# Performance work log

Measured on AMD Instinct MI355X. Metric: run time of the kernel, lower is better.

The kernel has to match this reference:

```python
import jax, jax.numpy as jnp
import numpy as np

N, A, MO, LX, H, S, P, B, BL = 64, 128, 126, 96, 1024, 32, 2, 16, 32
T = (B - 2) * BL
L = B * BL        # 512
IN = MO + A + LX + S      # 382: cat([mo, aud, lxm, style])
GIN = IN + H              # 1406: GRU input = cat([in_embed, mo, aud, lxm, style])

def gelu(x):
    return jax.nn.gelu(x, approximate=False)  # torch F.gelu default (erf)

def gru_cell(x, h, wih, whh, bih, bhh):
    # torch nn.GRU cell math
    gi = x @ wih + bih  # [N,3H]
    gh = h @ whh + bhh  # [N,3H]
    ir, iz, inn = jnp.split(gi, 3, axis=-1)
    hr, hz, hn = jnp.split(gh, 3, axis=-1)
    r = jax.nn.sigmoid(ir + hr)
    z = jax.nn.sigmoid(iz + hz)
    n = jnp.tanh(inn + r * hn)
    return (1.0 - z) * n + z * h

def layernorm(x, g, b, eps=1e-5):
    m = x.mean(-1, keepdims=True)
    v = x.var(-1, keepdims=True)
    return (x - m) * jax.lax.rsqrt(v + eps) * g + b

def setup_inputs():
    key = jax.random.key(0)
    k = jax.random.split(key, 20)
    f = jnp.float32
    def rn(i, shape, s=0.05):
        return jax.random.normal(k[i], shape, dtype=f) * s
    return dict(
        aud_embed=jax.random.normal(k[0], (N, A, T), f),
        mo=jax.random.normal(k[1], (N, MO, L), f),
        lxm=jax.random.normal(k[2], (N, LX, B), f),
        vid_indices=jax.random.randint(k[3], (N, B), 0, 5),
        eps=jax.random.normal(k[4], (T, N, S), f),
        csi_w0=rn(5, (MO + LX, H)), csi_b0=jnp.zeros((H,), f),
        csi_w1=rn(6, (H, H)), csi_b1=jnp.zeros((H,), f),
        csi_w2=rn(7, (H, H * P)), csi_b2=jnp.zeros((H * P,), f),
        spk_emb=rn(8, (5, S), 0.001),
        mu_w=rn(9, (S, S)), mu_b=jnp.zeros((S,), f),
        lv_w=rn(10, (S, S)), lv_b=jnp.zeros((S,), f),
        emb_in_w=rn(11, (IN, H)), emb_in_b=jnp.zeros((H,), f),
        wih0=rn(12, (GIN, 3 * H)), whh0=rn(13, (H, 3 * H)),
        bih0=jnp.zeros((3 * H,), f), bhh0=jnp.zeros((3 * H,), f),
        wih1=rn(14, (H, 3 * H)), whh1=rn(15, (H, 3 * H)),
        bih1=jnp.zeros((3 * H,), f), bhh1=jnp.zeros((3 * H,), f),
        ln_g=jnp.ones((H,), f), ln_b=jnp.zeros((H,), f),
        pred_w=rn(16, (H, MO), 0.02), pred_b=jnp.zeros((MO,), f),
    )

def reference(aud_embed, mo, lxm, vid_indices, eps,
              csi_w0, csi_b0, csi_w1, csi_b1, csi_w2, csi_b2,
              spk_emb, mu_w, mu_b, lv_w, lv_b,
              emb_in_w, emb_in_b,
              wih0, whh0, bih0, bhh0, wih1, whh1, bih1, bhh1,
              ln_g, ln_b, pred_w, pred_b):
    # CellStateInitializer(mo[:,:,BL-1], lxm[:,:,0]) -> [P, N, H]
    x = gelu(jnp.concatenate([mo[:, :, BL - 1], lxm[:, :, 0]], axis=-1) @ csi_w0 + csi_b0)
    x = gelu(x @ csi_w1 + csi_b1)
    x = (x @ csi_w2 + csi_b2).reshape(N, P, H)
    cell = jnp.transpose(x, (1, 0, 2))  # [P,N,H]

    blk = jnp.repeat(jnp.arange(B - 2), BL)            # [T] block index per frame
    aud_seq = jnp.transpose(aud_embed, (2, 0, 1))      # [T,N,A]
    lxm_seq = jnp.transpose(lxm, (2, 0, 1))[blk + 1]   # [T,N,LX]
    vid_seq = vid_indices.T[blk + 1]                   # [T,N]
    zc = spk_emb[vid_seq]                              # [T,N,S]
    z_mu = zc @ mu_w + mu_b                            # [T,N,S]
    z_lv = zc @ lv_w + lv_b                            # [T,N,S]
    style = z_mu + eps * jnp.exp(0.5 * z_lv)           # reparameterize, fresh eps each frame

    def step(carry, xs):
        pre_mo, h0, h1 = carry
        aud_t, lxm_t, st_t = xs
        xcat = jnp.concatenate([pre_mo, aud_t, lxm_t, st_t], axis=-1)  # [N,IN]
        ine = gelu(xcat @ emb_in_w + emb_in_b)                          # [N,H]
        gx = jnp.concatenate([ine, xcat], axis=-1)                      # [N,GIN]
        h0n = gru_cell(gx, h0, wih0, whh0, bih0, bhh0)
        h1n = gru_cell(h0n, h1, wih1, whh1, bih1, bhh1)
        out = layernorm(h1n, ln_g, ln_b)
        pred = out @ pred_w + pred_b                                    # [N,MO]
        return (pred, h0n, h1n), pred

    init = (mo[:, :, BL - 1], cell[0], cell[1])
    _, preds = jax.lax.scan(step, init, (aud_seq, lxm_seq, style))
    mo_hat = jnp.transpose(preds, (1, 2, 0))   # [N,MO,T]
    z_mu_hat = jnp.transpose(z_mu, (1, 2, 0))  # [N,S,T]
    z_lv_hat = jnp.transpose(z_lv, (1, 2, 0))  # [N,S,T]
    return mo_hat, z_mu_hat, z_lv_hat
```

## Files before the change

### kernel.cpp

```cpp
#include <hip/hip_runtime.h>
#include <cmath>

typedef _Float16 f16;
typedef _Float16 f16x8 __attribute__((ext_vector_type(8)));
typedef float f32x4 __attribute__((ext_vector_type(4)));
typedef unsigned long long u64;

#define MFMA_F16(a,b,c) __builtin_amdgcn_mfma_f32_16x16x32_f16((a),(b),(c),0,0,0)
#define AGENT __HIP_MEMORY_SCOPE_AGENT

#define TSTEPS 448
#define OFF_MU 3612672
#define OFF_LV 4530176
#define LDS_BYTES 156160

#define S1 0
#define S2 1
#define S3 2
#define S3B 3
#define S4 4
#define S4G 5

struct Ptrs {
  const float *aud, *mo, *lxm, *eps;
  const int *vid;
  const float *csi_w0, *csi_b0, *csi_w1, *csi_b1, *csi_w2, *csi_b2;
  const float *spk, *mu_w, *mu_b, *lv_w, *lv_b;
  const float *embW, *embB;
  const float *wih0, *whh0, *bih0, *bhh0;
  const float *wih1, *whh1, *bih1, *bhh1;
  const float *ln_g, *ln_b, *predW, *predB;
  float *out;
  unsigned *bar;
  float *part, *mu5, *lv5, *h0F, *h1F, *gsbs;
  f16 *h0B, *h1B, *ineB, *xcat;
  float *ghP0, *ghP1, *x0, *x1, *predsT;
  f16 *whh0P, *whh1P, *wih0aP, *wih0bP, *wih1P, *embWP, *predWP;
};

__device__ __forceinline__ float geluf(float x) {
  return 0.5f * x * (1.0f + erff(x * 0.7071067811865475f));
}
__device__ __forceinline__ float sigmf(float x) {
  return __builtin_amdgcn_rcpf(1.0f + __expf(-x));
}
__device__ __forceinline__ float tanhf_fast(float x) {
  float xc = fmaxf(x, -44.f);
  float e = __expf(-2.f * xc);
  return (1.f - e) * __builtin_amdgcn_rcpf(1.f + e);
}

__device__ __forceinline__ u64 ldc8(const void* p) {
  return __hip_atomic_load((const u64*)p, __ATOMIC_RELAXED, AGENT);
}
__device__ __forceinline__ void stc8(void* p, u64 v) {
  __hip_atomic_store((u64*)p, v, __ATOMIC_RELAXED, AGENT);
}
__device__ __forceinline__ void stcf(float* p, float v) {
  __hip_atomic_store(p, v, __ATOMIC_RELAXED, AGENT);
}
__device__ __forceinline__ f16x8 toH(u64 a, u64 b) {
  union { u64 u[2]; f16x8 h; } r; r.u[0] = a; r.u[1] = b; return r.h;
}
__device__ __forceinline__ f32x4 toF(u64 a, u64 b) {
  union { u64 u[2]; f32x4 f; } r; r.u[0] = a; r.u[1] = b; return r.f;
}
__device__ __forceinline__ u64 packF2(float a, float b) {
  union { float f[2]; u64 u; } r; r.f[0] = a; r.f[1] = b; return r.u;
}
__device__ __forceinline__ void st_pair(f16* base, float v, int lm, bool pred) {
  float vn = __shfl_xor(v, 1);
  if (!(lm & 1) && pred) {
    union { f16 h[2]; unsigned u; } pk;
    pk.h[0] = (f16)v; pk.h[1] = (f16)vn;
    __hip_atomic_store((unsigned*)base, pk.u, __ATOMIC_RELAXED, AGENT);
  }
}


__global__ void k_init(Ptrs p) {
  int gid = blockIdx.x * 256 + threadIdx.x;
  if (gid < 16384) p.bar[gid] = 0u;
}

__global__ void k_pack(const float* __restrict__ src, f16* __restrict__ dst,
                       int K, int rowOff, int realN, int ldN,
                       const float* __restrict__ scale) {
  int ct = blockIdx.x, kt = blockIdx.y;
  int e = threadIdx.x * 2;
  int l = e >> 3, i = e & 7;
  int k = kt * 32 + (l >> 4) * 8 + i;
  int col = ct * 16 + (l & 15);
  f16 v0 = (f16)0.f, v1 = (f16)0.f;
  if (k < K && col < realN) {
    float s = scale ? scale[rowOff + k] : 1.f;
    v0 = (f16)(src[(size_t)(rowOff + k) * ldN + col] * s);
  }
  if (k + 1 < K && col < realN) {
    float s = scale ? scale[rowOff + k + 1] : 1.f;
    v1 = (f16)(src[(size_t)(rowOff + k + 1) * ldN + col] * s);
  }
  size_t o = ((size_t)ct * gridDim.y + kt) * 512 + e;
  dst[o] = v0; dst[o + 1] = v1;
}

__global__ void k_gsbs(Ptrs p) {
  int c = threadIdx.x;
  if (c < 126) {
    float gs = 0.f, bs = 0.f;
    for (int k = 0; k < 1024; k++) {
      float w = p.predW[(size_t)k * 126 + c];
      gs += p.ln_g[k] * w;
      bs += p.ln_b[k] * w;
    }
    p.gsbs[c] = gs; p.gsbs[128 + c] = bs;
  }
}

__global__ void k_csi1(Ptrs p) {
  int gid = blockIdx.x * 256 + threadIdx.x;
  int n = gid >> 10, c = gid & 1023;
  float acc = p.csi_b0[c];
  const float* w = p.csi_w0 + c;
  for (int k = 0; k < 126; k++) acc += p.mo[((size_t)(n * 126 + k)) * 512 + 31] * w[(size_t)k * 1024];
  for (int k = 0; k < 96; k++)  acc += p.lxm[(size_t)(n * 96 + k) * 16] * w[(size_t)(126 + k) * 1024];
  p.x0[gid] = geluf(acc);
}

__global__ void k_csi2(Ptrs p) {
  int gid = blockIdx.x * 256 + threadIdx.x;
  int n = gid >> 10, c = gid & 1023;
  float acc = p.csi_b1[c];
  const float* w = p.csi_w1 + c;
  const float* x = p.x0 + (size_t)n * 1024;
  for (int k = 0; k < 1024; k++) acc += x[k] * w[(size_t)k * 1024];
  p.x1[gid] = geluf(acc);
}

__global__ void k_csi3(Ptrs p) {
  int gid = blockIdx.x * 256 + threadIdx.x;
  int n = gid >> 11, c2 = gid & 2047;
  float acc = p.csi_b2[c2];
  const float* w = p.csi_w2 + c2;
  const float* x = p.x1 + (size_t)n * 1024;
  for (int k = 0; k < 1024; k++) acc += x[k] * w[(size_t)k * 2048];
  if (c2 < 1024) { p.h0F[n * 1024 + c2] = acc; p.h0B[n * 1024 + c2] = (f16)acc; }
  else           { p.h1F[n * 1024 + c2 - 1024] = acc; p.h1B[n * 1024 + c2 - 1024] = (f16)acc; }
}

__global__ void k_gh(Ptrs p) {
  int gid = blockIdx.x * 256 + threadIdx.x;
  int which = gid >= 196608;
  int g2 = which ? gid - 196608 : gid;
  int n = g2 / 3072, c = g2 % 3072;
  const float* h = which ? p.h1F : p.h0F;
  const float* W = which ? p.whh1 : p.whh0;
  const float* bb = which ? p.bhh1 : p.bhh0;
  float acc = bb[c];
  const float* hr = h + (size_t)n * 1024;
  for (int k = 0; k < 1024; k++) acc += hr[k] * W[(size_t)k * 3072 + c];
  int g = c >> 10, col = c & 1023;
  int ct = col >> 4, lm = col & 15, w = n >> 4, lq = (n >> 2) & 3, r = n & 3;
  float* dst = which ? p.ghP1 : p.ghP0;
  dst[((size_t)((ct * 16 + lm) * 16 + w * 4 + lq)) * 16 + g * 4 + r] = acc;
}

__global__ void k_style1(Ptrs p) {
  int tid = threadIdx.x;
  if (tid < 160) {
    int v = tid >> 5, s = tid & 31;
    float m = p.mu_b[s], lv = p.lv_b[s];
    for (int k = 0; k < 32; k++) {
      float z = p.spk[v * 32 + k];
      m += z * p.mu_w[k * 32 + s];
      lv += z * p.lv_w[k * 32 + s];
    }
    p.mu5[v * 32 + s] = m; p.lv5[v * 32 + s] = lv;
  }
}

__global__ void k_style2(Ptrs p) {
  int gid = blockIdx.x * 256 + threadIdx.x;
  int t = gid % 448;
  int rr = gid / 448;
  int s = rr & 31, n = rr >> 5;
  int v = p.vid[n * 16 + (t >> 5) + 1];
  float mu = p.mu5[v * 32 + s], lv = p.lv5[v * 32 + s];
  float e = p.eps[((size_t)t * 64 + n) * 32 + s];
  float st = mu + e * expf(0.5f * lv);
  p.out[OFF_MU + ((size_t)n * 32 + s) * 448 + t] = mu;
  p.out[OFF_LV + ((size_t)n * 32 + s) * 448 + t] = lv;
  p.xcat[((size_t)t * 64 + n) * 384 + 350 + s] = (f16)st;
}

__global__ void k_aud(Ptrs p) {
  __shared__ float tile[32][65];
  int bid = blockIdx.x;
  int n = bid / 28, rem = bid % 28;
  int a0 = (rem / 7) * 32, t0 = (rem % 7) * 64;
  int tid = threadIdx.x;
  for (int i = tid; i < 2048; i += 256) {
    int ai = i >> 6, tj = i & 63;
    tile[ai][tj] = p.aud[((size_t)n * 128 + a0 + ai) * 448 + t0 + tj];
  }
  __syncthreads();
  for (int i = tid; i < 2048; i += 256) {
    int tj = i >> 5, ai = i & 31;
    p.xcat[((size_t)(t0 + tj) * 64 + n) * 384 + 126 + a0 + ai] = (f16)tile[ai][tj];
  }
}

__global__ void k_lxm(Ptrs p) {
  int gid = blockIdx.x * 256 + threadIdx.x;
  int l_ = gid % 96;
  int r = gid / 96;
  int n = r & 63, t = r >> 6;
  int tb = (t >> 5) + 1;
  p.xcat[((size_t)t * 64 + n) * 384 + 254 + l_] = (f16)p.lxm[((size_t)n * 96 + l_) * 16 + tb];
}

__global__ void k_premo0(Ptrs p) {
  int gid = blockIdx.x * 256 + threadIdx.x;
  if (gid < 8064) {
    int n = gid / 126, m = gid % 126;
    p.xcat[(size_t)n * 384 + m] = (f16)p.mo[((size_t)n * 126 + m) * 512 + 31];
  }
}

__global__ void k_padz(Ptrs p) {
  int gid = blockIdx.x * 256 + threadIdx.x;
  int t = gid >> 7, rem = gid & 127;
  int n = rem >> 1, c = 382 + (rem & 1);
  p.xcat[((size_t)t * 64 + n) * 384 + c] = (f16)0.f;
}


__device__ __forceinline__ void sigc(unsigned* bar, int cls, int idx, unsigned val) {
  asm volatile("s_waitcnt vmcnt(0)" ::: "memory");
  __syncthreads();
  if (threadIdx.x == 0)
    __hip_atomic_store(&bar[(cls * 64 + idx) * 32], val, __ATOMIC_RELAXED, AGENT);
}
__device__ __forceinline__ void waitc(unsigned* bar, int cls, unsigned tgt, int nsig) {
  if (threadIdx.x < (unsigned)nsig) {
    const unsigned* f = &bar[(cls * 64 + threadIdx.x) * 32];
    while (__hip_atomic_load(f, __ATOMIC_RELAXED, AGENT) < tgt) {}
  }
  __syncthreads();
}

__device__ __forceinline__ void gemm3(const f16* aRow, const f16* L, int l,
                                      f32x4& A0, f32x4& A1, f32x4& A2) {
  const f16* w0 = L + l * 8;
  u64 ua[16], ub[16];
  #pragma unroll
  for (int j = 0; j < 8; j++) { ua[2*j] = ldc8(aRow + j * 32); ua[2*j+1] = ldc8(aRow + j * 32 + 4); }
  #pragma unroll
  for (int j = 0; j < 8; j++) { ub[2*j] = ldc8(aRow + 256 + j * 32); ub[2*j+1] = ldc8(aRow + 256 + j * 32 + 4); }
  #pragma unroll
  for (int j = 0; j < 8; j++) {
    f16x8 av = toH(ua[2*j], ua[2*j+1]);
    A0 = MFMA_F16(av, *(const f16x8*)(w0 + j * 512), A0);
    A1 = MFMA_F16(av, *(const f16x8*)(w0 + 16384 + j * 512), A1);
    A2 = MFMA_F16(av, *(const f16x8*)(w0 + 32768 + j * 512), A2);
  }
  #pragma unroll
  for (int j = 0; j < 8; j++) { ua[2*j] = ldc8(aRow + 512 + j * 32); ua[2*j+1] = ldc8(aRow + 512 + j * 32 + 4); }
  #pragma unroll
  for (int j = 0; j < 8; j++) {
    f16x8 av = toH(ub[2*j], ub[2*j+1]);
    int kt = 8 + j;
    A0 = MFMA_F16(av, *(const f16x8*)(w0 + kt * 512), A0);
    A1 = MFMA_F16(av, *(const f16x8*)(w0 + 16384 + kt * 512), A1);
    A2 = MFMA_F16(av, *(const f16x8*)(w0 + 32768 + kt * 512), A2);
  }
  #pragma unroll
  for (int j = 0; j < 8; j++) { ub[2*j] = ldc8(aRow + 768 + j * 32); ub[2*j+1] = ldc8(aRow + 768 + j * 32 + 4); }
  #pragma unroll
  for (int j = 0; j < 8; j++) {
    f16x8 av = toH(ua[2*j], ua[2*j+1]);
    int kt = 16 + j;
    A0 = MFMA_F16(av, *(const f16x8*)(w0 + kt * 512), A0);
    A1 = MFMA_F16(av, *(const f16x8*)(w0 + 16384 + kt * 512), A1);
    A2 = MFMA_F16(av, *(const f16x8*)(w0 + 32768 + kt * 512), A2);
  }
  #pragma unroll
  for (int j = 0; j < 8; j++) {
    f16x8 av = toH(ub[2*j], ub[2*j+1]);
    int kt = 24 + j;
    A0 = MFMA_F16(av, *(const f16x8*)(w0 + kt * 512), A0);
    A1 = MFMA_F16(av, *(const f16x8*)(w0 + 16384 + kt * 512), A1);
    A2 = MFMA_F16(av, *(const f16x8*)(w0 + 32768 + kt * 512), A2);
  }
}

__global__ __launch_bounds__(256, 1) void k_scan(Ptrs p) {
  extern __shared__ char smem[];
  f16* L = (f16*)smem;
  const int b = blockIdx.x, tid = threadIdx.x;
  const int w = tid >> 6, l = tid & 63;
  const int lm = l & 15, lq = l >> 4;

  {
    auto cp = [&](int dstF16, const f16* src, int nF16) {
      uint4* d = (uint4*)smem + (dstF16 >> 3);
      const uint4* s = (const uint4*)src;
      for (int i = tid; i < (nF16 >> 3); i += 256) d[i] = s[i];
    };
    if (b < 64) {
      cp(0,     p.wih0aP + (size_t)b * 16384, 16384);
      cp(16384, p.wih0aP + (size_t)(64 + b) * 16384, 16384);
      cp(32768, p.wih0aP + (size_t)(128 + b) * 16384, 16384);
      cp(49152, p.wih0bP + (size_t)b * 6144, 6144);
      cp(55296, p.wih0bP + (size_t)(64 + b) * 6144, 6144);
      cp(61440, p.wih0bP + (size_t)(128 + b) * 6144, 6144);
    } else if (b < 128) {
      int cb = b - 64;
      cp(0,     p.wih1P + (size_t)cb * 16384, 16384);
      cp(16384, p.wih1P + (size_t)(64 + cb) * 16384, 16384);
      cp(32768, p.wih1P + (size_t)(128 + cb) * 16384, 16384);
      cp(49152, p.embWP + (size_t)cb * 6144, 6144);
      if (cb < 8) cp(55296, p.predWP + (size_t)cb * 16384, 16384);
    } else if (b < 192) {
      int i = b - 128;
      cp(0,     p.whh0P + (size_t)i * 16384, 16384);
      cp(16384, p.whh0P + (size_t)(64 + i) * 16384, 16384);
      cp(32768, p.whh0P + (size_t)(128 + i) * 16384, 16384);
    } else {
      int i = b - 192;
      cp(0,     p.whh1P + (size_t)i * 16384, 16384);
      cp(16384, p.whh1P + (size_t)(64 + i) * 16384, 16384);
      cp(32768, p.whh1P + (size_t)(128 + i) * 16384, 16384);
    }
  }
  float b0r = 0.f, b1r = 0.f, b2r = 0.f, ebr = 0.f, pbr = 0.f;
  float GsR = 0.f, BsR = 0.f;
  float hs[4] = {0.f, 0.f, 0.f, 0.f};
  if (b < 64) {
    int col = b * 16 + lm;
    b0r = p.bih0[col]; b1r = p.bih0[1024 + col]; b2r = p.bih0[2048 + col];
    #pragma unroll
    for (int r = 0; r < 4; r++) hs[r] = p.h0F[(size_t)(w * 16 + lq * 4 + r) * 1024 + col];
  } else if (b < 128) {
    int col = (b - 64) * 16 + lm;
    b0r = p.bih1[col]; b1r = p.bih1[1024 + col]; b2r = p.bih1[2048 + col];
    ebr = p.embB[col];
    #pragma unroll
    for (int r = 0; r < 4; r++) hs[r] = p.h1F[(size_t)(w * 16 + lq * 4 + r) * 1024 + col];
    if (b < 72 && col < 126) {
      pbr = p.predB[col];
      GsR = p.gsbs[col];
      BsR = p.gsbs[128 + col];
    }
  } else if (b < 192) {
    int col = (b - 128) * 16 + lm;
    b0r = p.bhh0[col]; b1r = p.bhh0[1024 + col]; b2r = p.bhh0[2048 + col];
  } else {
    int col = (b - 192) * 16 + lm;
    b0r = p.bhh1[col]; b1r = p.bhh1[1024 + col]; b2r = p.bhh1[2048 + col];
  }
  __syncthreads();

  unsigned* bar = p.bar;

  for (unsigned t = 0; t < TSTEPS; t++) {
    const f16* xc = p.xcat + (size_t)t * 24576;

    if (b < 64) {
      f32x4 a0 = {0,0,0,0}, a1 = {0,0,0,0}, a2 = {0,0,0,0};
      const f16* aB = xc + (w * 16 + lm) * 384 + lq * 8;
      const f16* wl = L + 49152 + l * 8;
      #pragma unroll
      for (int kt = 4; kt < 12; kt++) {
        f16x8 av = *(const f16x8*)(aB + kt * 32);
        a0 = MFMA_F16(av, *(const f16x8*)(wl + kt * 512), a0);
        a1 = MFMA_F16(av, *(const f16x8*)(wl + 6144 + kt * 512), a1);
        a2 = MFMA_F16(av, *(const f16x8*)(wl + 12288 + kt * 512), a2);
      }
      if (t) waitc(bar, S4, t, 8);
      f32x4 gip0, gip1, gip2;
      {
        u64 up[8];
        #pragma unroll
        for (int kt = 0; kt < 4; kt++) { up[2*kt] = ldc8(aB + kt * 32); up[2*kt+1] = ldc8(aB + kt * 32 + 4); }
        #pragma unroll
        for (int kt = 0; kt < 4; kt++) {
          f16x8 av = toH(up[2*kt], up[2*kt+1]);
          a0 = MFMA_F16(av, *(const f16x8*)(wl + kt * 512), a0);
          a1 = MFMA_F16(av, *(const f16x8*)(wl + 6144 + kt * 512), a1);
          a2 = MFMA_F16(av, *(const f16x8*)(wl + 12288 + kt * 512), a2);
        }
        #pragma unroll
        for (int r = 0; r < 4; r++) {
          gip0[r] = a0[r] + b0r; gip1[r] = a1[r] + b1r; gip2[r] = a2[r] + b2r;
        }
      }
      waitc(bar, S3B, t, 64);
      const float* rec = p.ghP0 + ((size_t)((b * 16 + lm) * 16 + w * 4 + lq)) * 16;
      u64 r0 = ldc8(rec), r1 = ldc8(rec + 2), r2 = ldc8(rec + 4);
      u64 r3 = ldc8(rec + 6), r4 = ldc8(rec + 8), r5 = ldc8(rec + 10);
      waitc(bar, S1, t + 1, 64);
      {
        f32x4 A0 = {0,0,0,0}, A1 = {0,0,0,0}, A2 = {0,0,0,0};
        gemm3(p.ineB + (w * 16 + lm) * 1024 + lq * 8, L, l, A0, A1, A2);
        f32x4 g0 = toF(r0, r1), g1 = toF(r2, r3), g2 = toF(r4, r5);
        int col = b * 16 + lm;
        #pragma unroll
        for (int r = 0; r < 4; r++) {
          int row = w * 16 + lq * 4 + r;
          float r_ = sigmf(A0[r] + gip0[r] + g0[r]);
          float z_ = sigmf(A1[r] + gip1[r] + g1[r]);
          float n_ = tanhf_fast(A2[r] + gip2[r] + r_ * g2[r]);
          float hn = (1.f - z_) * n_ + z_ * hs[r];
          hs[r] = hn;
          st_pair(p.h0B + (size_t)row * 1024 + col, hn, lm, true);
        }
      }
      sigc(bar, S2, b, t + 1);
    } else if (b < 128) {
      int cb = b - 64;
      int col = cb * 16 + lm;
      f32x4 acc = {0,0,0,0};
      const f16* aB = xc + (w * 16 + lm) * 384 + lq * 8;
      const f16* wl = L + 49152 + l * 8;
      #pragma unroll
      for (int kt = 4; kt < 12; kt++)
        acc = MFMA_F16(*(const f16x8*)(aB + kt * 32), *(const f16x8*)(wl + kt * 512), acc);
      if (t) waitc(bar, S4, t, 8);
      {
        u64 up[8];
        #pragma unroll
        for (int kt = 0; kt < 4; kt++) { up[2*kt] = ldc8(aB + kt * 32); up[2*kt+1] = ldc8(aB + kt * 32 + 4); }
        #pragma unroll
        for (int kt = 0; kt < 4; kt++)
          acc = MFMA_F16(toH(up[2*kt], up[2*kt+1]), *(const f16x8*)(wl + kt * 512), acc);
        #pragma unroll
        for (int r = 0; r < 4; r++) {
          int row = w * 16 + lq * 4 + r;
          float v = geluf(acc[r] + ebr);
          st_pair(p.ineB + (size_t)row * 1024 + col, v, lm, true);
        }
      }
      sigc(bar, S1, cb, t + 1);
      waitc(bar, S4G, t, 64);
      const float* rec = p.ghP1 + ((size_t)((cb * 16 + lm) * 16 + w * 4 + lq)) * 16;
      u64 r0 = ldc8(rec), r1 = ldc8(rec + 2), r2 = ldc8(rec + 4);
      u64 r3 = ldc8(rec + 6), r4 = ldc8(rec + 8), r5 = ldc8(rec + 10);
      waitc(bar, S2, t + 1, 64);
      {
        f32x4 A0 = {0,0,0,0}, A1 = {0,0,0,0}, A2 = {0,0,0,0};
        gemm3(p.h0B + (w * 16 + lm) * 1024 + lq * 8, L, l, A0, A1, A2);
        f32x4 g0 = toF(r0, r1), g1 = toF(r2, r3), g2 = toF(r4, r5);
        float sv[4], sq[4];
        #pragma unroll
        for (int r = 0; r < 4; r++) {
          int row = w * 16 + lq * 4 + r;
          float r_ = sigmf(A0[r] + b0r + g0[r]);
          float z_ = sigmf(A1[r] + b1r + g1[r]);
          float n_ = tanhf_fast(A2[r] + b2r + r_ * g2[r]);
          float hn = (1.f - z_) * n_ + z_ * hs[r];
          hs[r] = hn;
          st_pair(p.h1B + (size_t)row * 1024 + col, hn, lm, true);
          sv[r] = hn; sq[r] = hn * hn;
        }
        #pragma unroll
        for (int m = 1; m < 16; m <<= 1) {
          #pragma unroll
          for (int r = 0; r < 4; r++) { sv[r] += __shfl_xor(sv[r], m); sq[r] += __shfl_xor(sq[r], m); }
        }
        if (lm == 0) {
          #pragma unroll
          for (int r = 0; r < 4; r++) {
            int row = w * 16 + lq * 4 + r;
            stc8(&p.part[cb * 128 + row * 2], packF2(sv[r], sq[r]));
          }
        }
      }
      sigc(bar, S3, cb, t + 1);
      if (cb < 8) {
        waitc(bar, S3, t + 1, 64);
        float* redS = (float*)(smem + 151552);
        float* statsS = (float*)(smem + 155648);
        const f16* hB = p.h1B + (size_t)(w * 16 + lm) * 1024 + lq * 8;
        const f16* wp = L + 55296 + l * 8;
        u64 ua[16], ub[16];
        #pragma unroll
        for (int j = 0; j < 8; j++) { ua[2*j] = ldc8(hB + j * 32); ua[2*j+1] = ldc8(hB + j * 32 + 4); }
        #pragma unroll
        for (int j = 0; j < 8; j++) { ub[2*j] = ldc8(hB + 256 + j * 32); ub[2*j+1] = ldc8(hB + 256 + j * 32 + 4); }
        {
          int gg = tid >> 5, j4 = tid & 31;
          u64 pu[16];
          #pragma unroll
          for (int c = 0; c < 8; c++) {
            const float* q = p.part + ((gg * 8 + c) * 128 + j4 * 4);
            pu[2*c] = ldc8(q); pu[2*c+1] = ldc8(q + 2);
          }
          f32x4 s = {0,0,0,0};
          #pragma unroll
          for (int c = 0; c < 8; c++) s += toF(pu[2*c], pu[2*c+1]);
          *(f32x4*)(redS + gg * 128 + j4 * 4) = s;
        }
        __syncthreads();
        if (tid < 128) {
          float v = 0.f;
          #pragma unroll
          for (int gg = 0; gg < 8; gg++) v += redS[gg * 128 + tid];
          statsS[tid] = v;
        }
        __syncthreads();
        f32x4 pacc = {0,0,0,0};
        auto compP = [&](u64* cur, int g) {
          #pragma unroll
          for (int j = 0; j < 8; j++) {
            int kt = g * 8 + j;
            pacc = MFMA_F16(toH(cur[2*j], cur[2*j+1]), *(const f16x8*)(wp + kt * 512), pacc);
          }
        };
        compP(ua, 0);
        #pragma unroll
        for (int j = 0; j < 8; j++) { ua[2*j] = ldc8(hB + 512 + j * 32); ua[2*j+1] = ldc8(hB + 512 + j * 32 + 4); }
        compP(ub, 1);
        #pragma unroll
        for (int j = 0; j < 8; j++) { ub[2*j] = ldc8(hB + 768 + j * 32); ub[2*j+1] = ldc8(hB + 768 + j * 32 + 4); }
        compP(ua, 2);
        compP(ub, 3);
        #pragma unroll
        for (int r = 0; r < 4; r++) {
          int row = w * 16 + lq * 4 + r;
          float mean = statsS[row * 2] * 0.0009765625f;
          float var  = statsS[row * 2 + 1] * 0.0009765625f - mean * mean;
          float rstd = rsqrtf(var + 1e-5f);
          float v = rstd * (pacc[r] - mean * GsR) + BsR + pbr;
          if (col < 126) stcf(&p.predsT[(size_t)t * 8064 + row * 126 + col], v);
          st_pair(p.xcat + (size_t)(t + 1) * 24576 + row * 384 + col, v, lm,
                  col < 126 && t < 447);
        }
        sigc(bar, S4, cb, t + 1);
      }
    } else if (b < 192) {
      int i = b - 128;
      waitc(bar, S2, t + 1, 64);
      {
        f32x4 A0 = {0,0,0,0}, A1 = {0,0,0,0}, A2 = {0,0,0,0};
        gemm3(p.h0B + (w * 16 + lm) * 1024 + lq * 8, L, l, A0, A1, A2);
        float* rec = p.ghP0 + ((size_t)((i * 16 + lm) * 16 + w * 4 + lq)) * 16;
        stc8(rec,      packF2(A0[0] + b0r, A0[1] + b0r));
        stc8(rec + 2,  packF2(A0[2] + b0r, A0[3] + b0r));
        stc8(rec + 4,  packF2(A1[0] + b1r, A1[1] + b1r));
        stc8(rec + 6,  packF2(A1[2] + b1r, A1[3] + b1r));
        stc8(rec + 8,  packF2(A2[0] + b2r, A2[1] + b2r));
        stc8(rec + 10, packF2(A2[2] + b2r, A2[3] + b2r));
      }
      sigc(bar, S3B, i, t + 1);
    } else {
      int i = b - 192;
      waitc(bar, S3, t + 1, 64);
      {
        f32x4 A0 = {0,0,0,0}, A1 = {0,0,0,0}, A2 = {0,0,0,0};
        gemm3(p.h1B + (w * 16 + lm) * 1024 + lq * 8, L, l, A0, A1, A2);
        float* rec = p.ghP1 + ((size_t)((i * 16 + lm) * 16 + w * 4 + lq)) * 16;
        stc8(rec,      packF2(A0[0] + b0r, A0[1] + b0r));
        stc8(rec + 2,  packF2(A0[2] + b0r, A0[3] + b0r));
        stc8(rec + 4,  packF2(A1[0] + b1r, A1[1] + b1r));
        stc8(rec + 6,  packF2(A1[2] + b1r, A1[3] + b1r));
        stc8(rec + 8,  packF2(A2[0] + b2r, A2[1] + b2r));
        stc8(rec + 10, packF2(A2[2] + b2r, A2[3] + b2r));
      }
      sigc(bar, S4G, i, t + 1);
    }
  }

  waitc(bar, S4, TSTEPS, 8);
  {
    float* trS = (float*)smem;
    for (int g = b; g < 504; g += 256) {
      int p0 = g * 16;
      for (int t0 = 0; t0 < 448; t0 += 16) {
        int tc = tid >> 4, pp = tid & 15;
        trS[tc * 17 + pp] = p.predsT[(size_t)(t0 + tc) * 8064 + p0 + pp];
        __syncthreads();
        p.out[(size_t)(p0 + (tid >> 4)) * 448 + t0 + (tid & 15)] = trS[(tid & 15) * 17 + (tid >> 4)];
        __syncthreads();
      }
    }
  }
}


extern "C" void kernel_launch(void* const* d_in, const int* in_sizes, int n_in,
                              void* d_out, int out_size, void* d_ws, size_t ws_size,
                              hipStream_t stream) {
  Ptrs p;
  p.aud = (const float*)d_in[0];
  p.mo  = (const float*)d_in[1];
  p.lxm = (const float*)d_in[2];
  p.vid = (const int*)d_in[3];
  p.eps = (const float*)d_in[4];
  p.csi_w0 = (const float*)d_in[5];  p.csi_b0 = (const float*)d_in[6];
  p.csi_w1 = (const float*)d_in[7];  p.csi_b1 = (const float*)d_in[8];
  p.csi_w2 = (const float*)d_in[9];  p.csi_b2 = (const float*)d_in[10];
  p.spk  = (const float*)d_in[11];
  p.mu_w = (const float*)d_in[12];   p.mu_b = (const float*)d_in[13];
  p.lv_w = (const float*)d_in[14];   p.lv_b = (const float*)d_in[15];
  p.embW = (const float*)d_in[16];   p.embB = (const float*)d_in[17];
  p.wih0 = (const float*)d_in[18];   p.whh0 = (const float*)d_in[19];
  p.bih0 = (const float*)d_in[20];   p.bhh0 = (const float*)d_in[21];
  p.wih1 = (const float*)d_in[22];   p.whh1 = (const float*)d_in[23];
  p.bih1 = (const float*)d_in[24];   p.bhh1 = (const float*)d_in[25];
  p.ln_g = (const float*)d_in[26];   p.ln_b = (const float*)d_in[27];
  p.predW = (const float*)d_in[28];  p.predB = (const float*)d_in[29];
  p.out = (float*)d_out;

  char* ws = (char*)d_ws;
  size_t off = 0;
  auto al = [&](size_t bytes) -> void* {
    void* r = (void*)(ws + off);
    off += (bytes + 255) & ~(size_t)255;
    return r;
  };
  p.bar    = (unsigned*)al(65536);
  p.part   = (float*)al(32768);
  p.mu5    = (float*)al(640);
  p.lv5    = (float*)al(640);
  p.gsbs   = (float*)al(1024);
  p.h0F    = (float*)al(262144);
  p.h1F    = (float*)al(262144);
  p.h0B    = (f16*)al(131072);
  p.h1B    = (f16*)al(131072);
  p.ineB   = (f16*)al(131072);
  p.ghP0   = (float*)al(1048576);
  p.ghP1   = (float*)al(1048576);
  p.x0     = (float*)al(262144);
  p.x1     = (float*)al(262144);
  p.predsT = (float*)al(14450688);
  p.xcat   = (f16*)al(22020096);
  p.whh0P  = (f16*)al(6291456);
  p.whh1P  = (f16*)al(6291456);
  p.wih0aP = (f16*)al(6291456);
  p.wih0bP = (f16*)al(2359296);
  p.wih1P  = (f16*)al(6291456);
  p.embWP  = (f16*)al(786432);
  p.predWP = (f16*)al(262144);

  k_init<<<64, 256, 0, stream>>>(p);

  k_pack<<<dim3(192, 32), 256, 0, stream>>>(p.whh0, p.whh0P, 1024, 0, 3072, 3072, nullptr);
  k_pack<<<dim3(192, 32), 256, 0, stream>>>(p.whh1, p.whh1P, 1024, 0, 3072, 3072, nullptr);
  k_pack<<<dim3(192, 32), 256, 0, stream>>>(p.wih0, p.wih0aP, 1024, 0, 3072, 3072, nullptr);
  k_pack<<<dim3(192, 12), 256, 0, stream>>>(p.wih0, p.wih0bP, 382, 1024, 3072, 3072, nullptr);
  k_pack<<<dim3(192, 32), 256, 0, stream>>>(p.wih1, p.wih1P, 1024, 0, 3072, 3072, nullptr);
  k_pack<<<dim3(64, 12), 256, 0, stream>>>(p.embW, p.embWP, 382, 0, 1024, 1024, nullptr);
  k_pack<<<dim3(8, 32), 256, 0, stream>>>(p.predW, p.predWP, 1024, 0, 126, 126, p.ln_g);

  k_gsbs<<<1, 128, 0, stream>>>(p);
  k_csi1<<<256, 256, 0, stream>>>(p);
  k_csi2<<<256, 256, 0, stream>>>(p);
  k_csi3<<<512, 256, 0, stream>>>(p);
  k_gh<<<1536, 256, 0, stream>>>(p);
  k_style1<<<1, 256, 0, stream>>>(p);
  k_style2<<<3584, 256, 0, stream>>>(p);
  k_aud<<<1792, 256, 0, stream>>>(p);
  k_lxm<<<10752, 256, 0, stream>>>(p);
  k_premo0<<<32, 256, 0, stream>>>(p);
  k_padz<<<224, 256, 0, stream>>>(p);

  k_scan<<<256, 256, LDS_BYTES, stream>>>(p);

  (void)in_sizes; (void)n_in; (void)out_size; (void)ws_size;
}
```

Measured before the change: 15.04 ms.

## Distribute prediction projection across all layer-1 blocks with atomic partial sums

Removes the separate S4 stage, in which 8 blocks waited for the full h1 and computed the LayerNorm plus prediction GEMM. Each of the 64 layer-1 GRU blocks now multiplies its own 16-column slice of h1 by a K-slice of the pre-scaled predW and atomically adds partial prediction sums and LN statistics into a double-buffered predSum buffer. Consumers then apply the LayerNorm correction when building the next step's pre_mo input. This removes one global barrier stage from the serial per-step critical path. In exchange it adds many float atomics per step, plus a zeroing pass and a parity buffer to keep steps from overlapping.

```diff
diff --git a/kernel.cpp b/kernel.cpp
--- a/kernel.cpp
+++ b/kernel.cpp
@@ -14,12 +14,13 @@
 #define OFF_LV 4530176
 #define LDS_BYTES 156160
 
+#define PS_STRIDE 8320
+
 #define S1 0
 #define S2 1
 #define S3 2
 #define S3B 3
-#define S4 4
-#define S4G 5
+#define S4G 4
 
 struct Ptrs {
   const float *aud, *mo, *lxm, *eps;
@@ -32,10 +33,10 @@
   const float *ln_g, *ln_b, *predW, *predB;
   float *out;
   unsigned *bar;
-  float *part, *mu5, *lv5, *h0F, *h1F, *gsbs;
+  float *mu5, *lv5, *h0F, *h1F, *gsbs, *predSum;
   f16 *h0B, *h1B, *ineB, *xcat;
   float *ghP0, *ghP1, *x0, *x1, *predsT;
-  f16 *whh0P, *whh1P, *wih0aP, *wih0bP, *wih1P, *embWP, *predWP;
+  f16 *whh0P, *whh1P, *wih0aP, *wih0bP, *wih1P, *embWP, *predWKP;
 };
 
 __device__ __forceinline__ float geluf(float x) {
@@ -58,6 +59,12 @@
 }
 __device__ __forceinline__ void stcf(float* p, float v) {
   __hip_atomic_store(p, v, __ATOMIC_RELAXED, AGENT);
+}
+__device__ __forceinline__ float ldcf(const float* p) {
+  return __hip_atomic_load(p, __ATOMIC_RELAXED, AGENT);
+}
+__device__ __forceinline__ void fadd(float* p, float v) {
+  __hip_atomic_fetch_add(p, v, __ATOMIC_RELAXED, AGENT);
 }
 __device__ __forceinline__ f16x8 toH(u64 a, u64 b) {
   union { u64 u[2]; f16x8 h; } r; r.u[0] = a; r.u[1] = b; return r.h;
@@ -81,37 +88,51 @@
 __global__ void k_init(Ptrs p) {
   int gid = blockIdx.x * 256 + threadIdx.x;
   if (gid < 16384) p.bar[gid] = 0u;
+  int g2 = gid - 16384;
+  if (g2 >= 0 && g2 < 2 * PS_STRIDE) p.predSum[g2] = 0.f;
 }
 
 __global__ void k_pack(const float* __restrict__ src, f16* __restrict__ dst,
-                       int K, int rowOff, int realN, int ldN,
-                       const float* __restrict__ scale) {
+                       int K, int rowOff, int realN, int ldN) {
   int ct = blockIdx.x, kt = blockIdx.y;
   int e = threadIdx.x * 2;
   int l = e >> 3, i = e & 7;
   int k = kt * 32 + (l >> 4) * 8 + i;
   int col = ct * 16 + (l & 15);
   f16 v0 = (f16)0.f, v1 = (f16)0.f;
-  if (k < K && col < realN) {
-    float s = scale ? scale[rowOff + k] : 1.f;
-    v0 = (f16)(src[(size_t)(rowOff + k) * ldN + col] * s);
-  }
-  if (k + 1 < K && col < realN) {
-    float s = scale ? scale[rowOff + k + 1] : 1.f;
-    v1 = (f16)(src[(size_t)(rowOff + k + 1) * ldN + col] * s);
-  }
+  if (k < K && col < realN)     v0 = (f16)src[(size_t)(rowOff + k) * ldN + col];
+  if (k + 1 < K && col < realN) v1 = (f16)src[(size_t)(rowOff + k + 1) * ldN + col];
   size_t o = ((size_t)ct * gridDim.y + kt) * 512 + e;
   dst[o] = v0; dst[o + 1] = v1;
 }
 
+__global__ void k_packP(Ptrs p) {
+  int ct = blockIdx.x, cb = blockIdx.y;
+  int e = threadIdx.x * 2;
+  int l = e >> 3, i = e & 7;
+  int k = (l >> 4) * 8 + i;
+  int col = ct * 16 + (l & 15);
+  f16 v0 = (f16)0.f, v1 = (f16)0.f;
+  int kg = cb * 16 + k;
+  if (k < 16 && col < 126)
+    v0 = (f16)(p.predW[(size_t)kg * 126 + col] * p.ln_g[kg]);
+  if (k + 1 < 16 && col < 126)
+    v1 = (f16)(p.predW[(size_t)(kg + 1) * 126 + col] * p.ln_g[kg + 1]);
+  size_t o = ((size_t)cb * 8 + ct) * 512 + e;
+  p.predWKP[o] = v0; p.predWKP[o + 1] = v1;
+}
+
 __global__ void k_gsbs(Ptrs p) {
   int c = threadIdx.x;
-  if (c < 126) {
+  if (c < 128) {
     float gs = 0.f, bs = 0.f;
-    for (int k = 0; k < 1024; k++) {
-      float w = p.predW[(size_t)k * 126 + c];
-      gs += p.ln_g[k] * w;
-      bs += p.ln_b[k] * w;
+    if (c < 126) {
+      for (int k = 0; k < 1024; k++) {
+        float w = p.predW[(size_t)k * 126 + c];
+        gs += p.ln_g[k] * w;
+        bs += p.ln_b[k] * w;
+      }
+      bs += p.predB[c];
     }
     p.gsbs[c] = gs; p.gsbs[128 + c] = bs;
   }
@@ -249,6 +270,36 @@
   __syncthreads();
 }
 
+__device__ __forceinline__ void build_dyn(const float* pS, int R, int lq,
+                                          const float2* gsbsS, const f16* aB,
+                                          f16x8 av[4]) {
+  u64 sld = ldc8(pS + 8192 + R * 2);
+  u64 pv[16];
+  #pragma unroll
+  for (int kt = 0; kt < 4; kt++)
+    #pragma unroll
+    for (int q = 0; q < 4; q++)
+      pv[kt * 4 + q] = ldc8(pS + R * 128 + kt * 32 + lq * 8 + q * 2);
+  union { u64 u; float f[2]; } s; s.u = sld;
+  float mean = s.f[0] * 0.0009765625f;
+  float var  = s.f[1] * 0.0009765625f - mean * mean;
+  float rstd = rsqrtf(var + 1e-5f);
+  #pragma unroll
+  for (int kt = 0; kt < 4; kt++) {
+    #pragma unroll
+    for (int q = 0; q < 4; q++) {
+      union { u64 u; float f[2]; } pp; pp.u = pv[kt * 4 + q];
+      #pragma unroll
+      for (int h = 0; h < 2; h++) {
+        int c = kt * 32 + lq * 8 + q * 2 + h;
+        float2 gb = gsbsS[c];
+        av[kt][q * 2 + h] = (f16)(rstd * (pp.f[h] - mean * gb.x) + gb.y);
+      }
+    }
+  }
+  if (lq == 3) { av[3][6] = aB[3 * 32 + 6]; av[3][7] = aB[3 * 32 + 7]; }
+}
+
 __device__ __forceinline__ void gemm3(const f16* aRow, const f16* L, int l,
                                       f32x4& A0, f32x4& A1, f32x4& A2) {
   const f16* w0 = L + l * 8;
@@ -314,13 +365,19 @@
       cp(49152, p.wih0bP + (size_t)b * 6144, 6144);
       cp(55296, p.wih0bP + (size_t)(64 + b) * 6144, 6144);
       cp(61440, p.wih0bP + (size_t)(128 + b) * 6144, 6144);
+      float2* gsbsS = (float2*)(smem + 135168);
+      for (int i2 = tid; i2 < 128; i2 += 256)
+        gsbsS[i2] = make_float2(p.gsbs[i2], p.gsbs[128 + i2]);
     } else if (b < 128) {
       int cb = b - 64;
       cp(0,     p.wih1P + (size_t)cb * 16384, 16384);
       cp(16384, p.wih1P + (size_t)(64 + cb) * 16384, 16384);
       cp(32768, p.wih1P + (size_t)(128 + cb) * 16384, 16384);
       cp(49152, p.embWP + (size_t)cb * 6144, 6144);
-      if (cb < 8) cp(55296, p.predWP + (size_t)cb * 16384, 16384);
+      cp(55296, p.predWKP + (size_t)cb * 4096, 4096);
+      float2* gsbsS = (float2*)(smem + 118784);
+      for (int i2 = tid; i2 < 128; i2 += 256)
+        gsbsS[i2] = make_float2(p.gsbs[i2], p.gsbs[128 + i2]);
     } else if (b < 192) {
       int i = b - 128;
       cp(0,     p.whh0P + (size_t)i * 16384, 16384);
@@ -333,8 +390,8 @@
       cp(32768, p.whh1P + (size_t)(128 + i) * 16384, 16384);
     }
   }
-  float b0r = 0.f, b1r = 0.f, b2r = 0.f, ebr = 0.f, pbr = 0.f;
-  float GsR = 0.f, BsR = 0.f;
+  float b0r = 0.f, b1r = 0.f, b2r = 0.f, ebr = 0.f;
+  float GsR = 0.f, Bs2R = 0.f;
   float hs[4] = {0.f, 0.f, 0.f, 0.f};
   if (b < 64) {
     int col = b * 16 + lm;
@@ -347,17 +404,16 @@
     ebr = p.embB[col];
     #pragma unroll
     for (int r = 0; r < 4; r++) hs[r] = p.h1F[(size_t)(w * 16 + lq * 4 + r) * 1024 + col];
-    if (b < 72 && col < 126) {
-      pbr = p.predB[col];
-      GsR = p.gsbs[col];
-      BsR = p.gsbs[128 + col];
-    }
   } else if (b < 192) {
     int col = (b - 128) * 16 + lm;
     b0r = p.bhh0[col]; b1r = p.bhh0[1024 + col]; b2r = p.bhh0[2048 + col];
   } else {
     int col = (b - 192) * 16 + lm;
     b0r = p.bhh1[col]; b1r = p.bhh1[1024 + col]; b2r = p.bhh1[2048 + col];
+    if (b < 200) {
+      int pc = (b - 192) * 16 + lm;
+      if (pc < 126) { GsR = p.gsbs[pc]; Bs2R = p.gsbs[128 + pc]; }
+    }
   }
   __syncthreads();
 
@@ -377,18 +433,22 @@
         a1 = MFMA_F16(av, *(const f16x8*)(wl + 6144 + kt * 512), a1);
         a2 = MFMA_F16(av, *(const f16x8*)(wl + 12288 + kt * 512), a2);
       }
-      if (t) waitc(bar, S4, t, 8);
+      if (t) waitc(bar, S3, t, 64);
       f32x4 gip0, gip1, gip2;
       {
-        u64 up[8];
-        #pragma unroll
-        for (int kt = 0; kt < 4; kt++) { up[2*kt] = ldc8(aB + kt * 32); up[2*kt+1] = ldc8(aB + kt * 32 + 4); }
+        f16x8 av[4];
+        if (t == 0) {
+          #pragma unroll
+          for (int kt = 0; kt < 4; kt++) av[kt] = *(const f16x8*)(aB + kt * 32);
+        } else {
+          build_dyn(p.predSum + ((t + 1) & 1) * PS_STRIDE, w * 16 + lm, lq,
+                    (const float2*)(smem + 135168), aB, av);
+        }
         #pragma unroll
         for (int kt = 0; kt < 4; kt++) {
-          f16x8 av = toH(up[2*kt], up[2*kt+1]);
-          a0 = MFMA_F16(av, *(const f16x8*)(wl + kt * 512), a0);
-          a1 = MFMA_F16(av, *(const f16x8*)(wl + 6144 + kt * 512), a1);
-          a2 = MFMA_F16(av, *(const f16x8*)(wl + 12288 + kt * 512), a2);
+          a0 = MFMA_F16(av[kt], *(const f16x8*)(wl + kt * 512), a0);
+          a1 = MFMA_F16(av[kt], *(const f16x8*)(wl + 6144 + kt * 512), a1);
+          a2 = MFMA_F16(av[kt], *(const f16x8*)(wl + 12288 + kt * 512), a2);
         }
         #pragma unroll
         for (int r = 0; r < 4; r++) {
@@ -426,14 +486,19 @@
       #pragma unroll
       for (int kt = 4; kt < 12; kt++)
         acc = MFMA_F16(*(const f16x8*)(aB + kt * 32), *(const f16x8*)(wl + kt * 512), acc);
-      if (t) waitc(bar, S4, t, 8);
+      if (t) waitc(bar, S3, t, 64);
       {
-        u64 up[8];
-        #pragma unroll
-        for (int kt = 0; kt < 4; kt++) { up[2*kt] = ldc8(aB + kt * 32); up[2*kt+1] = ldc8(aB + kt * 32 + 4); }
+        f16x8 av[4];
+        if (t == 0) {
+          #pragma unroll
+          for (int kt = 0; kt < 4; kt++) av[kt] = *(const f16x8*)(aB + kt * 32);
+        } else {
+          build_dyn(p.predSum + ((t + 1) & 1) * PS_STRIDE, w * 16 + lm, lq,
+                    (const float2*)(smem + 118784), aB, av);
+        }
         #pragma unroll
         for (int kt = 0; kt < 4; kt++)
-          acc = MFMA_F16(toH(up[2*kt], up[2*kt+1]), *(const f16x8*)(wl + kt * 512), acc);
+          acc = MFMA_F16(av[kt], *(const f16x8*)(wl + kt * 512), acc);
         #pragma unroll
         for (int r = 0; r < 4; r++) {
           int row = w * 16 + lq * 4 + r;
@@ -452,6 +517,7 @@
         gemm3(p.h0B + (w * 16 + lm) * 1024 + lq * 8, L, l, A0, A1, A2);
         f32x4 g0 = toF(r0, r1), g1 = toF(r2, r3), g2 = toF(r4, r5);
         float sv[4], sq[4];
+        f16* sW = (f16*)(smem + 119808) + w * 256;
         #pragma unroll
         for (int r = 0; r < 4; r++) {
           int row = w * 16 + lq * 4 + r;
@@ -460,6 +526,7 @@
           float n_ = tanhf_fast(A2[r] + b2r + r_ * g2[r]);
           float hn = (1.f - z_) * n_ + z_ * hs[r];
           hs[r] = hn;
+          sW[(lq * 4 + r) * 16 + lm] = (f16)hn;
           st_pair(p.h1B + (size_t)row * 1024 + col, hn, lm, true);
           sv[r] = hn; sq[r] = hn * hn;
         }
@@ -468,76 +535,27 @@
           #pragma unroll
           for (int r = 0; r < 4; r++) { sv[r] += __shfl_xor(sv[r], m); sq[r] += __shfl_xor(sq[r], m); }
         }
+        float* pSw = p.predSum + (t & 1) * PS_STRIDE;
         if (lm == 0) {
           #pragma unroll
           for (int r = 0; r < 4; r++) {
-            int row = w * 16 + lq * 4 + r;
-            stc8(&p.part[cb * 128 + row * 2], packF2(sv[r], sq[r]));
+            fadd(pSw + 8192 + (w * 16 + lq * 4 + r) * 2,     sv[r]);
+            fadd(pSw + 8192 + (w * 16 + lq * 4 + r) * 2 + 1, sq[r]);
           }
         }
+        f16x8 pav = toH(0ull, 0ull);
+        if (lq < 2) pav = *(const f16x8*)(sW + lm * 16 + lq * 8);
+        const f16* Lpk = L + 55296 + l * 8;
+        #pragma unroll
+        for (int ct = 0; ct < 8; ct++) {
+          f32x4 pc = {0,0,0,0};
+          pc = MFMA_F16(pav, *(const f16x8*)(Lpk + ct * 512), pc);
+          #pragma unroll
+          for (int r = 0; r < 4; r++)
+            fadd(pSw + (w * 16 + lq * 4 + r) * 128 + ct * 16 + lm, pc[r]);
+        }
       }
       sigc(bar, S3, cb, t + 1);
-      if (cb < 8) {
-        waitc(bar, S3, t + 1, 64);
-        float* redS = (float*)(smem + 151552);
-        float* statsS = (float*)(smem + 155648);
-        const f16* hB = p.h1B + (size_t)(w * 16 + lm) * 1024 + lq * 8;
-        const f16* wp = L + 55296 + l * 8;
-        u64 ua[16], ub[16];
-        #pragma unroll
-        for (int j = 0; j < 8; j++) { ua[2*j] = ldc8(hB + j * 32); ua[2*j+1] = ldc8(hB + j * 32 + 4); }
-        #pragma unroll
-        for (int j = 0; j < 8; j++) { ub[2*j] = ldc8(hB + 256 + j * 32); ub[2*j+1] = ldc8(hB + 256 + j * 32 + 4); }
-        {
-          int gg = tid >> 5, j4 = tid & 31;
-          u64 pu[16];
-          #pragma unroll
-          for (int c = 0; c < 8; c++) {
-            const float* q = p.part + ((gg * 8 + c) * 128 + j4 * 4);
-            pu[2*c] = ldc8(q); pu[2*c+1] = ldc8(q + 2);
-          }
-          f32x4 s = {0,0,0,0};
-          #pragma unroll
-          for (int c = 0; c < 8; c++) s += toF(pu[2*c], pu[2*c+1]);
-          *(f32x4*)(redS + gg * 128 + j4 * 4) = s;
-        }
-        __syncthreads();
-        if (tid < 128) {
-          float v = 0.f;
-          #pragma unroll
-          for (int gg = 0; gg < 8; gg++) v += redS[gg * 128 + tid];
-          statsS[tid] = v;
-        }
-        __syncthreads();
-        f32x4 pacc = {0,0,0,0};
-        auto compP = [&](u64* cur, int g) {
-          #pragma unroll
-          for (int j = 0; j < 8; j++) {
-            int kt = g * 8 + j;
-            pacc = MFMA_F16(toH(cur[2*j], cur[2*j+1]), *(const f16x8*)(wp + kt * 512), pacc);
-          }
-        };
-        compP(ua, 0);
-        #pragma unroll
-        for (int j = 0; j < 8; j++) { ua[2*j] = ldc8(hB + 512 + j * 32); ua[2*j+1] = ldc8(hB + 512 + j * 32 + 4); }
-        compP(ub, 1);
-        #pragma unroll
-        for (int j = 0; j < 8; j++) { ub[2*j] = ldc8(hB + 768 + j * 32); ub[2*j+1] = ldc8(hB + 768 + j * 32 + 4); }
-        compP(ua, 2);
-        compP(ub, 3);
-        #pragma unroll
-        for (int r = 0; r < 4; r++) {
-          int row = w * 16 + lq * 4 + r;
-          float mean = statsS[row * 2] * 0.0009765625f;
-          float var  = statsS[row * 2 + 1] * 0.0009765625f - mean * mean;
-          float rstd = rsqrtf(var + 1e-5f);
-          float v = rstd * (pacc[r] - mean * GsR) + BsR + pbr;
-          if (col < 126) stcf(&p.predsT[(size_t)t * 8064 + row * 126 + col], v);
-          st_pair(p.xcat + (size_t)(t + 1) * 24576 + row * 384 + col, v, lm,
-                  col < 126 && t < 447);
-        }
-        sigc(bar, S4, cb, t + 1);
-      }
     } else if (b < 192) {
       int i = b - 128;
       waitc(bar, S2, t + 1, 64);
@@ -567,11 +585,32 @@
         stc8(rec + 8,  packF2(A2[0] + b2r, A2[1] + b2r));
         stc8(rec + 10, packF2(A2[2] + b2r, A2[3] + b2r));
       }
+      if (i < 8) {
+        const float* pSr = p.predSum + (t & 1) * PS_STRIDE;
+        int pc = i * 16 + lm;
+        if (pc < 126) {
+          #pragma unroll
+          for (int r = 0; r < 4; r++) {
+            int row = w * 16 + lq * 4 + r;
+            float raw = ldcf(pSr + row * 128 + pc);
+            union { u64 u; float f[2]; } ss; ss.u = ldc8(pSr + 8192 + row * 2);
+            float mean = ss.f[0] * 0.0009765625f;
+            float var  = ss.f[1] * 0.0009765625f - mean * mean;
+            float rstd = rsqrtf(var + 1e-5f);
+            stcf(&p.predsT[(size_t)t * 8064 + row * 126 + pc],
+                 rstd * (raw - mean * GsR) + Bs2R);
+          }
+        }
+      }
+      {
+        float* zp = p.predSum + ((t + 1) & 1) * PS_STRIDE + i * 130;
+        if (tid < 65) stc8(zp + tid * 2, 0ull);
+      }
       sigc(bar, S4G, i, t + 1);
     }
   }
 
-  waitc(bar, S4, TSTEPS, 8);
+  waitc(bar, S4G, TSTEPS, 64);
   {
     float* trS = (float*)smem;
     for (int g = b; g < 504; g += 256) {
@@ -619,39 +658,39 @@
     off += (bytes + 255) & ~(size_t)255;
     return r;
   };
-  p.bar    = (unsigned*)al(65536);
-  p.part   = (float*)al(32768);
-  p.mu5    = (float*)al(640);
-  p.lv5    = (float*)al(640);
-  p.gsbs   = (float*)al(1024);
-  p.h0F    = (float*)al(262144);
-  p.h1F    = (float*)al(262144);
-  p.h0B    = (f16*)al(131072);
-  p.h1B    = (f16*)al(131072);
-  p.ineB   = (f16*)al(131072);
-  p.ghP0   = (float*)al(1048576);
-  p.ghP1   = (float*)al(1048576);
-  p.x0     = (float*)al(262144);
-  p.x1     = (float*)al(262144);
-  p.predsT = (float*)al(14450688);
-  p.xcat   = (f16*)al(22020096);
-  p.whh0P  = (f16*)al(6291456);
-  p.whh1P  = (f16*)al(6291456);
-  p.wih0aP = (f16*)al(6291456);
-  p.wih0bP = (f16*)al(2359296);
-  p.wih1P  = (f16*)al(6291456);
-  p.embWP  = (f16*)al(786432);
-  p.predWP = (f16*)al(262144);
-
-  k_init<<<64, 256, 0, stream>>>(p);
-
-  k_pack<<<dim3(192, 32), 256, 0, stream>>>(p.whh0, p.whh0P, 1024, 0, 3072, 3072, nullptr);
-  k_pack<<<dim3(192, 32), 256, 0, stream>>>(p.whh1, p.whh1P, 1024, 0, 3072, 3072, nullptr);
-  k_pack<<<dim3(192, 32), 256, 0, stream>>>(p.wih0, p.wih0aP, 1024, 0, 3072, 3072, nullptr);
-  k_pack<<<dim3(192, 12), 256, 0, stream>>>(p.wih0, p.wih0bP, 382, 1024, 3072, 3072, nullptr);
-  k_pack<<<dim3(192, 32), 256, 0, stream>>>(p.wih1, p.wih1P, 1024, 0, 3072, 3072, nullptr);
-  k_pack<<<dim3(64, 12), 256, 0, stream>>>(p.embW, p.embWP, 382, 0, 1024, 1024, nullptr);
-  k_pack<<<dim3(8, 32), 256, 0, stream>>>(p.predW, p.predWP, 1024, 0, 126, 126, p.ln_g);
+  p.bar     = (unsigned*)al(65536);
+  p.predSum = (float*)al(66560);
+  p.mu5     = (float*)al(640);
+  p.lv5     = (float*)al(640);
+  p.gsbs    = (float*)al(1024);
+  p.h0F     = (float*)al(262144);
+  p.h1F     = (float*)al(262144);
+  p.h0B     = (f16*)al(131072);
+  p.h1B     = (f16*)al(131072);
+  p.ineB    = (f16*)al(131072);
+  p.ghP0    = (float*)al(1048576);
+  p.ghP1    = (float*)al(1048576);
+  p.x0      = (float*)al(262144);
+  p.x1      = (float*)al(262144);
+  p.predsT  = (float*)al(14450688);
+  p.xcat    = (f16*)al(22020096);
+  p.whh0P   = (f16*)al(6291456);
+  p.whh1P   = (f16*)al(6291456);
+  p.wih0aP  = (f16*)al(6291456);
+  p.wih0bP  = (f16*)al(2359296);
+  p.wih1P   = (f16*)al(6291456);
+  p.embWP   = (f16*)al(786432);
+  p.predWKP = (f16*)al(524288);
+
+  k_init<<<129, 256, 0, stream>>>(p);
+
+  k_pack<<<dim3(192, 32), 256, 0, stream>>>(p.whh0, p.whh0P, 1024, 0, 3072, 3072);
+  k_pack<<<dim3(192, 32), 256, 0, stream>>>(p.whh1, p.whh1P, 1024, 0, 3072, 3072);
+  k_pack<<<dim3(192, 32), 256, 0, stream>>>(p.wih0, p.wih0aP, 1024, 0, 3072, 3072);
+  k_pack<<<dim3(192, 12), 256, 0, stream>>>(p.wih0, p.wih0bP, 382, 1024, 3072, 3072);
+  k_pack<<<dim3(192, 32), 256, 0, stream>>>(p.wih1, p.wih1P, 1024, 0, 3072, 3072);
+  k_pack<<<dim3(64, 12), 256, 0, stream>>>(p.embW, p.embWP, 382, 0, 1024, 1024);
+  k_packP<<<dim3(8, 64), 256, 0, stream>>>(p);
 
   k_gsbs<<<1, 128, 0, stream>>>(p);
   k_csi1<<<256, 256, 0, stream>>>(p);
```

Result: slower. 16.73 ms (+11.2%).
